# Performance work log

Hardware: AMD Instinct MI355X
Metric: run time of the kernel (lower is better)

## Reference

```python
import jax, jax.numpy as jnp
import numpy as np

D = 1024
H = 16
DK = D // H


def apply_rope(x):
    # x: [B, H, T, dk]; interleaved-pair RoPE as in the torch source
    T, dim = x.shape[-2], x.shape[-1]
    inv_freq = 1.0 / (10000.0 ** (jnp.arange(0, dim, 2, dtype=x.dtype) / dim))  # [dk/2]
    pos = jnp.arange(T, dtype=x.dtype)
    sinusoid = pos[:, None] * inv_freq[None, :]  # [T, dk/2]
    sin, cos = jnp.sin(sinusoid), jnp.cos(sinusoid)
    x1, x2 = x[..., ::2], x[..., 1::2]
    rot = jnp.stack([x1 * cos - x2 * sin, x1 * sin + x2 * cos], axis=-1)
    return rot.reshape(x.shape)


def setup_inputs() -> dict:
    key = jax.random.key(0)
    k1, k2, k3, k4, k5 = jax.random.split(key, 5)
    B, T = 2, 2048
    s = 1.0 / np.sqrt(D)
    return {
        "x": jax.random.normal(k1, (B, T, D), dtype=jnp.float32),
        "W_qkv": jax.random.normal(k2, (D, 3 * D), dtype=jnp.float32) * s,
        "b_qkv": jnp.zeros((3 * D,), dtype=jnp.float32),
        "W_out": jax.random.normal(k3, (D, D), dtype=jnp.float32) * s,
        "b_out": jnp.zeros((D,), dtype=jnp.float32),
    }


def reference(x, W_qkv, b_qkv, W_out, b_out):
    B, T, C = x.shape
    qkv = x @ W_qkv + b_qkv  # [B, T, 3D]
    qkv = qkv.reshape(B, T, 3, H, DK).transpose(2, 0, 3, 1, 4)  # [3, B, H, T, dk]
    q, k, v = qkv[0], qkv[1], qkv[2]
    q, k = apply_rope(q), apply_rope(k)
    scores = jnp.einsum("bhtd,bhsd->bhts", q, k) / jnp.sqrt(jnp.asarray(DK, x.dtype))
    causal = jnp.tril(jnp.ones((T, T), dtype=bool))
    scores = jnp.where(causal, scores, jnp.asarray(-1e9, x.dtype))
    probs = jax.nn.softmax(scores, axis=-1)
    attn = jnp.einsum("bhts,bhsd->bhtd", probs, v)  # [B, H, T, dk]
    out = attn.transpose(0, 2, 1, 3).reshape(B, T, C)  # b h t d -> b t (h d)
    return out @ W_out + b_out
```

## Files before the change

### kernel.cpp

```cpp
#include <hip/hip_runtime.h>
#include <math.h>

#define DMODEL 1024
#define NHEAD  16
#define HDK    64
#define BATCH  2
#define SEQ    2048
#define MROWS  (BATCH*SEQ)
#define NQKV   (3*DMODEL)
#define LOG2_10000 13.287712379549449f
#define INV2PI 0.15915494309189535f
#define SCALE_LOG2E 0.1803368801111137f
#define M_FIX 8.0f

typedef __attribute__((ext_vector_type(8))) short bf16x8;
typedef __attribute__((ext_vector_type(4))) short s16x4;
typedef __attribute__((ext_vector_type(4))) float f32x4;
typedef __attribute__((ext_vector_type(2))) unsigned int u32x2;

__device__ __forceinline__ short f2bf(float f) {
    union { float f; unsigned u; } v; v.f = f;
    unsigned r = v.u + 0x7fffu + ((v.u >> 16) & 1u);
    return (short)(r >> 16);
}

__device__ __forceinline__ float fast_exp2(float x) {
#if __has_builtin(__builtin_amdgcn_exp2f)
    return __builtin_amdgcn_exp2f(x);
#else
    return exp2f(x);
#endif
}

__device__ __forceinline__ void gld_lds16(const short* g, short* l) {
    __builtin_amdgcn_global_load_lds(
        (const __attribute__((address_space(1))) void*)g,
        (__attribute__((address_space(3))) void*)l, 16, 0, 0);
}

__global__ __launch_bounds__(256) void prep_kernel(
    const float* __restrict__ x, const float* __restrict__ wqkv,
    const float* __restrict__ wout,
    short* __restrict__ xb, short* __restrict__ wqkv_t, short* __restrict__ wout_t,
    float2* __restrict__ rope)
{
    __shared__ __align__(16) short tile[32][36];
    const int tid = threadIdx.x;
    if (blockIdx.x < 2048) {
        const int i = (blockIdx.x * 256 + tid) * 8;
        float4 a = *(const float4*)(x + i);
        float4 b = *(const float4*)(x + i + 4);
        bf16x8 o;
        o[0] = f2bf(a.x); o[1] = f2bf(a.y); o[2] = f2bf(a.z); o[3] = f2bf(a.w);
        o[4] = f2bf(b.x); o[5] = f2bf(b.y); o[6] = f2bf(b.z); o[7] = f2bf(b.w);
        *(bf16x8*)(xb + i) = o;
        return;
    }
    if (blockIdx.x >= 2048 + 4096) {
        const int idx = (blockIdx.x - 6144) * 256 + tid;
        const int t = idx >> 5, f = idx & 31;
        const float invf = INV2PI * exp2f(-((float)f / 32.f) * LOG2_10000);
        const float rev = (float)t * invf;
        const float fr = rev - floorf(rev);
        float2 cs;
        cs.x = __builtin_amdgcn_cosf(fr);
        cs.y = __builtin_amdgcn_sinf(fr);
        rope[idx] = cs;
        return;
    }
    const int bx = blockIdx.x - 2048;
    int nx = bx & 127;
    const int ky = bx >> 7;
    const float* in; short* out; int N;
    if (nx < 96) { in = wqkv; out = wqkv_t; N = NQKV; }
    else         { in = wout; out = wout_t; N = DMODEL; nx -= 96; }
    const int n0 = nx * 32, k0 = ky * 32;
    {
        const int kr = tid >> 3, nc4 = tid & 7;
        float4 v = *(const float4*)&in[(size_t)(k0 + kr) * N + n0 + nc4 * 4];
        tile[nc4 * 4 + 0][kr] = f2bf(v.x);
        tile[nc4 * 4 + 1][kr] = f2bf(v.y);
        tile[nc4 * 4 + 2][kr] = f2bf(v.z);
        tile[nc4 * 4 + 3][kr] = f2bf(v.w);
    }
    __syncthreads();
    {
        const int nr = tid >> 3, kc4 = tid & 7;
        *(s16x4*)&out[(size_t)(n0 + nr) * DMODEL + k0 + kc4 * 4] =
            *(const s16x4*)&tile[nr][kc4 * 4];
    }
}

__global__ __launch_bounds__(256) void qkv_gemm_kernel(
    const short* __restrict__ xb, const short* __restrict__ Wt,
    const float* __restrict__ bias, const float2* __restrict__ rope,
    short* __restrict__ qd, short* __restrict__ kd, short* __restrict__ vtb)
{
    __shared__ __align__(16) short As[3][128 * 32];
    __shared__ __align__(16) short Bs[3][128 * 32];
    const int tid = threadIdx.x;
    const int lane = tid & 63, wave = tid >> 6;
    const int wm = wave & 1, wn = wave >> 1;
    const int l15 = lane & 15, quad = lane >> 4;
    const int n0 = blockIdx.x * 128, m0 = blockIdx.y * 128;
    const int srow = lane >> 2, sc = lane & 3;
    const int scp = sc ^ ((srow >> 1) & 3);
    const int rdx = (l15 >> 1) & 3;

    const short* gA1 = xb + (size_t)(m0 + wave * 32 + srow) * DMODEL + scp * 8;
    const short* gA2 = gA1 + (size_t)16 * DMODEL;
    const short* gB1 = Wt + (size_t)(n0 + wave * 32 + srow) * DMODEL + scp * 8;
    const short* gB2 = gB1 + (size_t)16 * DMODEL;
    const int lofsA1 = (wave * 32) * 32;
    const int lofsA2 = (wave * 32 + 16) * 32;

    f32x4 zero = {0.f, 0.f, 0.f, 0.f};
    f32x4 acc[4][4];
    #pragma unroll
    for (int i = 0; i < 4; ++i)
        #pragma unroll
        for (int j = 0; j < 4; ++j) acc[i][j] = zero;

#define QKV_COMPUTE(CUR)                                                          \
    {                                                                             \
        bf16x8 af[4], bfr[4];                                                     \
        _Pragma("unroll")                                                         \
        for (int i = 0; i < 4; ++i)                                               \
            af[i] = *(const bf16x8*)&As[CUR][(wm * 64 + i * 16 + l15) * 32 + (quad ^ rdx) * 8]; \
        _Pragma("unroll")                                                         \
        for (int j = 0; j < 4; ++j)                                               \
            bfr[j] = *(const bf16x8*)&Bs[CUR][(wn * 64 + j * 16 + l15) * 32 + (quad ^ rdx) * 8]; \
        _Pragma("unroll")                                                         \
        for (int i = 0; i < 4; ++i)                                               \
            _Pragma("unroll")                                                     \
            for (int j = 0; j < 4; ++j)                                           \
                acc[i][j] = __builtin_amdgcn_mfma_f32_16x16x32_bf16(af[i], bfr[j], acc[i][j], 0, 0, 0); \
    }

    gld_lds16(gA1, &As[0][lofsA1]);
    gld_lds16(gA2, &As[0][lofsA2]);
    gld_lds16(gB1, &Bs[0][lofsA1]);
    gld_lds16(gB2, &Bs[0][lofsA2]);
    gld_lds16(gA1 + 32, &As[1][lofsA1]);
    gld_lds16(gA2 + 32, &As[1][lofsA2]);
    gld_lds16(gB1 + 32, &Bs[1][lofsA1]);
    gld_lds16(gB2 + 32, &Bs[1][lofsA2]);

    int cur = 0, nx = 2;
    #pragma unroll 3
    for (int k = 0; k < 30; ++k) {
        const int kn = (k + 2) * 32;
        gld_lds16(gA1 + kn, &As[nx][lofsA1]);
        gld_lds16(gA2 + kn, &As[nx][lofsA2]);
        gld_lds16(gB1 + kn, &Bs[nx][lofsA1]);
        gld_lds16(gB2 + kn, &Bs[nx][lofsA2]);
        asm volatile("s_waitcnt vmcnt(8)\n\ts_barrier" ::: "memory");
        QKV_COMPUTE(cur);
        asm volatile("s_barrier" ::: "memory");
        cur = (cur == 2) ? 0 : cur + 1;
        nx  = (nx == 2) ? 0 : nx + 1;
    }
    asm volatile("s_waitcnt vmcnt(4)\n\ts_barrier" ::: "memory");
    QKV_COMPUTE(cur);
    cur = (cur == 2) ? 0 : cur + 1;
    asm volatile("s_waitcnt vmcnt(0)\n\ts_barrier" ::: "memory");
    QKV_COMPUTE(cur);
#undef QKV_COMPUTE

    const int which = n0 >> 10;
    float biasv[4];
    int hh[4], dd[4];
    #pragma unroll
    for (int j = 0; j < 4; ++j) {
        const int n = n0 + wn * 64 + j * 16 + l15;
        biasv[j] = bias[n];
        hh[j] = (n & 1023) >> 6;
        dd[j] = n & 63;
    }
    #pragma unroll
    for (int i = 0; i < 4; ++i) {
        const int mb = m0 + wm * 64 + i * 16 + quad * 4;
        const int b = mb >> 11, tb = mb & (SEQ - 1);
        if (which < 2) {
            #pragma unroll
            for (int j = 0; j < 4; ++j) {
                const int fj = dd[j] >> 1;
                #pragma unroll
                for (int r = 0; r < 4; ++r) {
                    const int t = tb + r;
                    float val = acc[i][j][r] + biasv[j];
                    const float2 cs = rope[t * 32 + fj];
                    const float partner = __shfl_xor(val, 1);
                    val = (lane & 1) ? (partner * cs.y + val * cs.x)
                                     : (val * cs.x - partner * cs.y);
                    short* dst = (which == 0) ? qd : kd;
                    dst[((size_t)(b * NHEAD + hh[j]) * SEQ + t) * HDK + dd[j]] = f2bf(val);
                }
            }
        } else {
            #pragma unroll
            for (int j = 0; j < 4; ++j) {
                s16x4 sv;
                #pragma unroll
                for (int r = 0; r < 4; ++r)
                    sv[r] = f2bf(acc[i][j][r] + biasv[j]);
                *(s16x4*)&vtb[((size_t)(b * NHEAD + hh[j]) * HDK + dd[j]) * SEQ + tb] = sv;
            }
        }
    }
}

__global__ __launch_bounds__(512) void attn_mfma_kernel(
    const short* __restrict__ qd, const short* __restrict__ kd,
    const short* __restrict__ vt, short* __restrict__ od)
{
    __shared__ __align__(16) short Ks[2][2][64 * 32];
    __shared__ __align__(16) short Vs[2][2][64 * 32];
    __shared__ __align__(16) short Ps[8][16 * 64];
    const int tid = threadIdx.x, lane = tid & 63, w = tid >> 6;
    const int l15 = lane & 15, quad = lane >> 4;
    const int par = w >> 2;
    const int ws = w & 3;
    const int id = (int)blockIdx.x;
    const int c = id & 7, g = id >> 3;
    const int qt = 31 - (g >> 2);
    const int jj = g & 3;
    const int hb = c + 8 * jj;
    const int h = hb & 15, b = hb >> 4;
    const size_t base = ((size_t)(b * NHEAD + h)) * SEQ * HDK;
    const int stid = tid & 255;
    const int hi = tid >> 8;
    const int srow = stid >> 2, sc = stid & 3;
    const int lofs = srow * 32 + (sc ^ ((srow >> 1) & 3)) * 8;
    const int rdx = (l15 >> 1) & 3;
    const int pmask = (l15 & 3) << 2;
    f32x4 zero = {0.f, 0.f, 0.f, 0.f};

    const short* kp = kd + base + (size_t)(hi * 64 + srow) * HDK + sc * 8;
    const short* vp = vt + base + (size_t)srow * SEQ + hi * 64 + sc * 8;

    const int q0 = qt * 64;
    const int trow = q0 + ws * 16 + l15;
    bf16x8 qf[2];
    {
        const short* qrow = qd + base + (size_t)trow * HDK;
        qf[0] = *(const bf16x8*)(qrow + quad * 8);
        qf[1] = *(const bf16x8*)(qrow + 32 + quad * 8);
    }
    float l_acc = 0.f;
    f32x4 o[4];
    #pragma unroll
    for (int j = 0; j < 4; ++j) o[j] = zero;

    const int nkt = qt + 1;
    const int npair = (nkt + 1) >> 1;
    short* myPs = &Ps[w][0];

    bf16x8 rk[2], rv[2];
    rk[0] = *(const bf16x8*)kp; rk[1] = *(const bf16x8*)(kp + 32);
    rv[0] = *(const bf16x8*)vp; rv[1] = *(const bf16x8*)(vp + 32);

    for (int p = 0; p < npair; ++p) {
        __syncthreads();
        *(bf16x8*)&Ks[hi][0][lofs] = rk[0];
        *(bf16x8*)&Ks[hi][1][lofs] = rk[1];
        *(bf16x8*)&Vs[hi][0][lofs] = rv[0];
        *(bf16x8*)&Vs[hi][1][lofs] = rv[1];
        __syncthreads();
        if (p + 1 < npair) {
            const int sn = (2 * p + 2) * 64;
            const short* kn = kp + (size_t)sn * HDK;
            const short* vn = vp + sn;
            rk[0] = *(const bf16x8*)kn; rk[1] = *(const bf16x8*)(kn + 32);
            rv[0] = *(const bf16x8*)vn; rv[1] = *(const bf16x8*)(vn + 32);
        }

        const int kt = 2 * p + par;
        if (kt < nkt) {
            f32x4 sacc[4];
            #pragma unroll
            for (int j = 0; j < 4; ++j) {
                const int ro = (j * 16 + l15) * 32 + (quad ^ rdx) * 8;
                bf16x8 kf0 = *(const bf16x8*)&Ks[par][0][ro];
                bf16x8 kf1 = *(const bf16x8*)&Ks[par][1][ro];
                sacc[j] = __builtin_amdgcn_mfma_f32_16x16x32_bf16(kf0, qf[0], zero, 0, 0, 0);
                sacc[j] = __builtin_amdgcn_mfma_f32_16x16x32_bf16(kf1, qf[1], sacc[j], 0, 0, 0);
            }
            if (kt == nkt - 1) {
                const int s0 = kt * 64;
                #pragma unroll
                for (int j = 0; j < 4; ++j) {
                    float pv[4];
                    #pragma unroll
                    for (int r = 0; r < 4; ++r) {
                        const int scol = s0 + j * 16 + quad * 4 + r;
                        const float sv = sacc[j][r] * SCALE_LOG2E - M_FIX;
                        pv[r] = (scol > trow) ? 0.f : fast_exp2(sv);
                        l_acc += pv[r];
                    }
                    unsigned pk0, pk1;
                    asm("v_cvt_pk_bf16_f32 %0, %1, %2" : "=v"(pk0) : "v"(pv[0]), "v"(pv[1]));
                    asm("v_cvt_pk_bf16_f32 %0, %1, %2" : "=v"(pk1) : "v"(pv[2]), "v"(pv[3]));
                    const int cc = (j * 4 + quad) ^ pmask;
                    u32x2 pkv = {pk0, pk1};
                    *(u32x2*)&myPs[l15 * 64 + cc * 4] = pkv;
                }
            } else {
                #pragma unroll
                for (int j = 0; j < 4; ++j) {
                    float pv[4];
                    #pragma unroll
                    for (int r = 0; r < 4; ++r) {
                        pv[r] = fast_exp2(sacc[j][r] * SCALE_LOG2E - M_FIX);
                        l_acc += pv[r];
                    }
                    unsigned pk0, pk1;
                    asm("v_cvt_pk_bf16_f32 %0, %1, %2" : "=v"(pk0) : "v"(pv[0]), "v"(pv[1]));
                    asm("v_cvt_pk_bf16_f32 %0, %1, %2" : "=v"(pk1) : "v"(pv[2]), "v"(pv[3]));
                    const int cc = (j * 4 + quad) ^ pmask;
                    u32x2 pkv = {pk0, pk1};
                    *(u32x2*)&myPs[l15 * 64 + cc * 4] = pkv;
                }
            }
            bf16x8 pf0 = *(const bf16x8*)&myPs[l15 * 64 + ((quad * 2) ^ pmask) * 4];
            bf16x8 pf1 = *(const bf16x8*)&myPs[l15 * 64 + ((8 + quad * 2) ^ pmask) * 4];
            #pragma unroll
            for (int j = 0; j < 4; ++j) {
                const int ro = (j * 16 + l15) * 32 + (quad ^ rdx) * 8;
                bf16x8 vf0 = *(const bf16x8*)&Vs[par][0][ro];
                bf16x8 vf1 = *(const bf16x8*)&Vs[par][1][ro];
                o[j] = __builtin_amdgcn_mfma_f32_16x16x32_bf16(pf0, vf0, o[j], 0, 0, 0);
                o[j] = __builtin_amdgcn_mfma_f32_16x16x32_bf16(pf1, vf1, o[j], 0, 0, 0);
            }
        }
    }

    float sr = l_acc;
    sr += __shfl_xor(sr, 16);
    sr += __shfl_xor(sr, 32);

    __syncthreads();
    float* ob   = (float*)&Ks[0][0][0];
    float* lbuf = (float*)&Vs[0][0][0];
    lbuf[w * 16 + l15] = sr;
    if (par == 1) {
        const int bi = (ws * 64 + lane) * 16;
        #pragma unroll
        for (int j = 0; j < 4; ++j)
            #pragma unroll
            for (int r = 0; r < 4; ++r) ob[bi + j * 4 + r] = o[j][r];
    }
    __syncthreads();
    if (par == 0) {
        const int bi = (ws * 64 + lane) * 16;
        #pragma unroll
        for (int j = 0; j < 4; ++j)
            #pragma unroll
            for (int r = 0; r < 4; ++r) o[j][r] += ob[bi + j * 4 + r];

        #pragma unroll
        for (int r = 0; r < 4; ++r) {
            const int qq = quad * 4 + r;
            const float lt = lbuf[ws * 16 + qq] + lbuf[(ws + 4) * 16 + qq];
            const float inv = 1.f / lt;
            const int t = q0 + ws * 16 + qq;
            #pragma unroll
            for (int j = 0; j < 4; ++j)
                od[((size_t)(b * SEQ + t) * NHEAD + h) * HDK + j * 16 + l15] =
                    f2bf(o[j][r] * inv);
        }
    }
}

__global__ __launch_bounds__(256) void out_gemm_kernel(
    const short* __restrict__ Ab, const short* __restrict__ Wt,
    const float* __restrict__ bias, float* __restrict__ out)
{
    __shared__ __align__(16) short As[2][128 * 32];
    __shared__ __align__(16) short Bs[2][64 * 32];
    const int tid = threadIdx.x;
    const int lane = tid & 63, wave = tid >> 6;
    const int wm = wave & 1, wn = wave >> 1;
    const int l15 = lane & 15, quad = lane >> 4;
    const int n0 = blockIdx.x * 64, m0 = blockIdx.y * 128;
    const int srow = lane >> 2, sc = lane & 3;
    const int scp = sc ^ ((srow >> 1) & 3);
    const int rdx = (l15 >> 1) & 3;

    const short* gA1 = Ab + (size_t)(m0 + wave * 32 + srow) * DMODEL + scp * 8;
    const short* gA2 = gA1 + (size_t)16 * DMODEL;
    const short* gB1 = Wt + (size_t)(n0 + wave * 16 + srow) * DMODEL + scp * 8;
    const int lofsA1 = (wave * 32) * 32;
    const int lofsA2 = (wave * 32 + 16) * 32;
    const int lofsB  = (wave * 16) * 32;

    f32x4 zero = {0.f, 0.f, 0.f, 0.f};
    f32x4 acc[4][2];
    #pragma unroll
    for (int i = 0; i < 4; ++i)
        #pragma unroll
        for (int j = 0; j < 2; ++j) acc[i][j] = zero;

    gld_lds16(gA1, &As[0][lofsA1]);
    gld_lds16(gA2, &As[0][lofsA2]);
    gld_lds16(gB1, &Bs[0][lofsB]);
    __syncthreads();

    for (int k = 0; k < DMODEL / 32; ++k) {
        const int cur = k & 1;
        if (k + 1 < DMODEL / 32) {
            const int kn = (k + 1) * 32;
            gld_lds16(gA1 + kn, &As[cur ^ 1][lofsA1]);
            gld_lds16(gA2 + kn, &As[cur ^ 1][lofsA2]);
            gld_lds16(gB1 + kn, &Bs[cur ^ 1][lofsB]);
        }
        bf16x8 af[4], bfr[2];
        #pragma unroll
        for (int i = 0; i < 4; ++i)
            af[i] = *(const bf16x8*)&As[cur][(wm * 64 + i * 16 + l15) * 32 + (quad ^ rdx) * 8];
        #pragma unroll
        for (int j = 0; j < 2; ++j)
            bfr[j] = *(const bf16x8*)&Bs[cur][(wn * 32 + j * 16 + l15) * 32 + (quad ^ rdx) * 8];
        #pragma unroll
        for (int i = 0; i < 4; ++i)
            #pragma unroll
            for (int j = 0; j < 2; ++j)
                acc[i][j] = __builtin_amdgcn_mfma_f32_16x16x32_bf16(af[i], bfr[j], acc[i][j], 0, 0, 0);
        __syncthreads();
    }

    #pragma unroll
    for (int j = 0; j < 2; ++j) {
        const int n = n0 + wn * 32 + j * 16 + l15;
        const float bv = bias[n];
        #pragma unroll
        for (int i = 0; i < 4; ++i)
            #pragma unroll
            for (int r = 0; r < 4; ++r) {
                const int m = m0 + wm * 64 + i * 16 + quad * 4 + r;
                out[(size_t)m * DMODEL + n] = acc[i][j][r] + bv;
            }
    }
}

extern "C" void kernel_launch(void* const* d_in, const int* in_sizes, int n_in,
                              void* d_out, int out_size, void* d_ws, size_t ws_size,
                              hipStream_t stream) {
    const float* x    = (const float*)d_in[0];
    const float* Wqkv = (const float*)d_in[1];
    const float* bqkv = (const float*)d_in[2];
    const float* Wout = (const float*)d_in[3];
    const float* bout = (const float*)d_in[4];
    float* out = (float*)d_out;

    short* ws = (short*)d_ws;
    short* xb     = ws;
    short* wqkv_t = xb + (size_t)4 * 1024 * 1024;
    short* wout_t = wqkv_t + (size_t)3 * 1024 * 1024;
    short* qd     = wout_t + (size_t)1024 * 1024;
    short* kd     = qd + (size_t)4 * 1024 * 1024;
    short* vtb    = kd + (size_t)4 * 1024 * 1024;
    short* attn   = vtb + (size_t)4 * 1024 * 1024;
    float2* rope  = (float2*)(attn + (size_t)4 * 1024 * 1024);

    prep_kernel<<<2048 + 4096 + 256, 256, 0, stream>>>(
        x, Wqkv, Wout, xb, wqkv_t, wout_t, rope);

    qkv_gemm_kernel<<<dim3(NQKV / 128, MROWS / 128), 256, 0, stream>>>(
        xb, wqkv_t, bqkv, rope, qd, kd, vtb);

    attn_mfma_kernel<<<1024, 512, 0, stream>>>(qd, kd, vtb, attn);

    out_gemm_kernel<<<dim3(DMODEL / 64, MROWS / 128), 256, 0, stream>>>(
        attn, wout_t, bout, out);
}
```

Measured before the change: 185.3 us.

## Widen K tile to 64 with double buffering in QKV and output GEMMs

Result: faster. 181.4 us (-2.1%).

```diff
diff --git a/kernel.cpp b/kernel.cpp
--- a/kernel.cpp
+++ b/kernel.cpp
@@ -96,23 +96,20 @@
     const float* __restrict__ bias, const float2* __restrict__ rope,
     short* __restrict__ qd, short* __restrict__ kd, short* __restrict__ vtb)
 {
-    __shared__ __align__(16) short As[3][128 * 32];
-    __shared__ __align__(16) short Bs[3][128 * 32];
+    __shared__ __align__(16) short As[2][128 * 64];
+    __shared__ __align__(16) short Bs[2][128 * 64];
     const int tid = threadIdx.x;
     const int lane = tid & 63, wave = tid >> 6;
     const int wm = wave & 1, wn = wave >> 1;
     const int l15 = lane & 15, quad = lane >> 4;
     const int n0 = blockIdx.x * 128, m0 = blockIdx.y * 128;
-    const int srow = lane >> 2, sc = lane & 3;
-    const int scp = sc ^ ((srow >> 1) & 3);
-    const int rdx = (l15 >> 1) & 3;
-
-    const short* gA1 = xb + (size_t)(m0 + wave * 32 + srow) * DMODEL + scp * 8;
-    const short* gA2 = gA1 + (size_t)16 * DMODEL;
-    const short* gB1 = Wt + (size_t)(n0 + wave * 32 + srow) * DMODEL + scp * 8;
-    const short* gB2 = gB1 + (size_t)16 * DMODEL;
-    const int lofsA1 = (wave * 32) * 32;
-    const int lofsA2 = (wave * 32 + 16) * 32;
+    const int srow = tid >> 3, sch = tid & 7;
+    const int schg = sch ^ (srow & 7);
+    const int lofs = srow * 64 + sch * 8;
+    const int rsw = l15 & 7;
+
+    const short* gA = xb + (size_t)(m0 + srow) * DMODEL + schg * 8;
+    const short* gB = Wt + (size_t)(n0 + srow) * DMODEL + schg * 8;
 
     f32x4 zero = {0.f, 0.f, 0.f, 0.f};
     f32x4 acc[4][4];
@@ -121,50 +118,52 @@
         #pragma unroll
         for (int j = 0; j < 4; ++j) acc[i][j] = zero;
 
-#define QKV_COMPUTE(CUR)                                                          \
-    {                                                                             \
-        bf16x8 af[4], bfr[4];                                                     \
-        _Pragma("unroll")                                                         \
-        for (int i = 0; i < 4; ++i)                                               \
-            af[i] = *(const bf16x8*)&As[CUR][(wm * 64 + i * 16 + l15) * 32 + (quad ^ rdx) * 8]; \
-        _Pragma("unroll")                                                         \
-        for (int j = 0; j < 4; ++j)                                               \
-            bfr[j] = *(const bf16x8*)&Bs[CUR][(wn * 64 + j * 16 + l15) * 32 + (quad ^ rdx) * 8]; \
-        _Pragma("unroll")                                                         \
-        for (int i = 0; i < 4; ++i)                                               \
-            _Pragma("unroll")                                                     \
-            for (int j = 0; j < 4; ++j)                                           \
-                acc[i][j] = __builtin_amdgcn_mfma_f32_16x16x32_bf16(af[i], bfr[j], acc[i][j], 0, 0, 0); \
-    }
-
-    gld_lds16(gA1, &As[0][lofsA1]);
-    gld_lds16(gA2, &As[0][lofsA2]);
-    gld_lds16(gB1, &Bs[0][lofsA1]);
-    gld_lds16(gB2, &Bs[0][lofsA2]);
-    gld_lds16(gA1 + 32, &As[1][lofsA1]);
-    gld_lds16(gA2 + 32, &As[1][lofsA2]);
-    gld_lds16(gB1 + 32, &Bs[1][lofsA1]);
-    gld_lds16(gB2 + 32, &Bs[1][lofsA2]);
-
-    int cur = 0, nx = 2;
-    #pragma unroll 3
-    for (int k = 0; k < 30; ++k) {
-        const int kn = (k + 2) * 32;
-        gld_lds16(gA1 + kn, &As[nx][lofsA1]);
-        gld_lds16(gA2 + kn, &As[nx][lofsA2]);
-        gld_lds16(gB1 + kn, &Bs[nx][lofsA1]);
-        gld_lds16(gB2 + kn, &Bs[nx][lofsA2]);
-        asm volatile("s_waitcnt vmcnt(8)\n\ts_barrier" ::: "memory");
+#define QKV_STAGE(BUF, KT)                                                     \
+    _Pragma("unroll")                                                          \
+    for (int r_ = 0; r_ < 4; ++r_) {                                           \
+        gld_lds16(gA + (size_t)(KT) * 64 + (size_t)(r_ * 32) * DMODEL,         \
+                  &As[BUF][r_ * 2048 + lofs]);                                 \
+        gld_lds16(gB + (size_t)(KT) * 64 + (size_t)(r_ * 32) * DMODEL,         \
+                  &Bs[BUF][r_ * 2048 + lofs]);                                 \
+    }
+
+#define QKV_COMPUTE(BUF)                                                       \
+    {                                                                          \
+        bf16x8 af[4][2], bfr[4][2];                                            \
+        _Pragma("unroll")                                                      \
+        for (int i = 0; i < 4; ++i) {                                          \
+            const int ra = (wm * 64 + i * 16 + l15) * 64;                      \
+            af[i][0] = *(const bf16x8*)&As[BUF][ra + (quad ^ rsw) * 8];        \
+            af[i][1] = *(const bf16x8*)&As[BUF][ra + ((4 + quad) ^ rsw) * 8];  \
+        }                                                                      \
+        _Pragma("unroll")                                                      \
+        for (int j = 0; j < 4; ++j) {                                          \
+            const int rb = (wn * 64 + j * 16 + l15) * 64;                      \
+            bfr[j][0] = *(const bf16x8*)&Bs[BUF][rb + (quad ^ rsw) * 8];       \
+            bfr[j][1] = *(const bf16x8*)&Bs[BUF][rb + ((4 + quad) ^ rsw) * 8]; \
+        }                                                                      \
+        _Pragma("unroll")                                                      \
+        for (int i = 0; i < 4; ++i)                                            \
+            _Pragma("unroll")                                                  \
+            for (int j = 0; j < 4; ++j) {                                      \
+                acc[i][j] = __builtin_amdgcn_mfma_f32_16x16x32_bf16(           \
+                    af[i][0], bfr[j][0], acc[i][j], 0, 0, 0);                  \
+                acc[i][j] = __builtin_amdgcn_mfma_f32_16x16x32_bf16(           \
+                    af[i][1], bfr[j][1], acc[i][j], 0, 0, 0);                  \
+            }                                                                  \
+    }
+
+    QKV_STAGE(0, 0);
+    asm volatile("s_waitcnt vmcnt(0)\n\ts_barrier" ::: "memory");
+
+    #pragma unroll 2
+    for (int kt = 0; kt < 16; ++kt) {
+        const int cur = kt & 1;
+        if (kt + 1 < 16) QKV_STAGE(cur ^ 1, kt + 1);
         QKV_COMPUTE(cur);
-        asm volatile("s_barrier" ::: "memory");
-        cur = (cur == 2) ? 0 : cur + 1;
-        nx  = (nx == 2) ? 0 : nx + 1;
-    }
-    asm volatile("s_waitcnt vmcnt(4)\n\ts_barrier" ::: "memory");
-    QKV_COMPUTE(cur);
-    cur = (cur == 2) ? 0 : cur + 1;
-    asm volatile("s_waitcnt vmcnt(0)\n\ts_barrier" ::: "memory");
-    QKV_COMPUTE(cur);
+        asm volatile("s_waitcnt vmcnt(0) lgkmcnt(0)\n\ts_barrier" ::: "memory");
+    }
+#undef QKV_STAGE
 #undef QKV_COMPUTE
 
     const int which = n0 >> 10;
@@ -376,23 +375,20 @@
     const short* __restrict__ Ab, const short* __restrict__ Wt,
     const float* __restrict__ bias, float* __restrict__ out)
 {
-    __shared__ __align__(16) short As[2][128 * 32];
-    __shared__ __align__(16) short Bs[2][64 * 32];
+    __shared__ __align__(16) short As[2][128 * 64];
+    __shared__ __align__(16) short Bs[2][64 * 64];
     const int tid = threadIdx.x;
     const int lane = tid & 63, wave = tid >> 6;
     const int wm = wave & 1, wn = wave >> 1;
     const int l15 = lane & 15, quad = lane >> 4;
     const int n0 = blockIdx.x * 64, m0 = blockIdx.y * 128;
-    const int srow = lane >> 2, sc = lane & 3;
-    const int scp = sc ^ ((srow >> 1) & 3);
-    const int rdx = (l15 >> 1) & 3;
-
-    const short* gA1 = Ab + (size_t)(m0 + wave * 32 + srow) * DMODEL + scp * 8;
-    const short* gA2 = gA1 + (size_t)16 * DMODEL;
-    const short* gB1 = Wt + (size_t)(n0 + wave * 16 + srow) * DMODEL + scp * 8;
-    const int lofsA1 = (wave * 32) * 32;
-    const int lofsA2 = (wave * 32 + 16) * 32;
-    const int lofsB  = (wave * 16) * 32;
+    const int srow = tid >> 3, sch = tid & 7;
+    const int schg = sch ^ (srow & 7);
+    const int lofs = srow * 64 + sch * 8;
+    const int rsw = l15 & 7;
+
+    const short* gA = Ab + (size_t)(m0 + srow) * DMODEL + schg * 8;
+    const short* gB = Wt + (size_t)(n0 + srow) * DMODEL + schg * 8;
 
     f32x4 zero = {0.f, 0.f, 0.f, 0.f};
     f32x4 acc[4][2];
@@ -401,33 +397,56 @@
         #pragma unroll
         for (int j = 0; j < 2; ++j) acc[i][j] = zero;
 
-    gld_lds16(gA1, &As[0][lofsA1]);
-    gld_lds16(gA2, &As[0][lofsA2]);
-    gld_lds16(gB1, &Bs[0][lofsB]);
-    __syncthreads();
-
-    for (int k = 0; k < DMODEL / 32; ++k) {
-        const int cur = k & 1;
-        if (k + 1 < DMODEL / 32) {
-            const int kn = (k + 1) * 32;
-            gld_lds16(gA1 + kn, &As[cur ^ 1][lofsA1]);
-            gld_lds16(gA2 + kn, &As[cur ^ 1][lofsA2]);
-            gld_lds16(gB1 + kn, &Bs[cur ^ 1][lofsB]);
-        }
-        bf16x8 af[4], bfr[2];
-        #pragma unroll
-        for (int i = 0; i < 4; ++i)
-            af[i] = *(const bf16x8*)&As[cur][(wm * 64 + i * 16 + l15) * 32 + (quad ^ rdx) * 8];
-        #pragma unroll
-        for (int j = 0; j < 2; ++j)
-            bfr[j] = *(const bf16x8*)&Bs[cur][(wn * 32 + j * 16 + l15) * 32 + (quad ^ rdx) * 8];
-        #pragma unroll
-        for (int i = 0; i < 4; ++i)
-            #pragma unroll
-            for (int j = 0; j < 2; ++j)
-                acc[i][j] = __builtin_amdgcn_mfma_f32_16x16x32_bf16(af[i], bfr[j], acc[i][j], 0, 0, 0);
-        __syncthreads();
-    }
+#define OUT_STAGE(BUF, KT)                                                     \
+    {                                                                          \
+        _Pragma("unroll")                                                      \
+        for (int r_ = 0; r_ < 4; ++r_)                                         \
+            gld_lds16(gA + (size_t)(KT) * 64 + (size_t)(r_ * 32) * DMODEL,     \
+                      &As[BUF][r_ * 2048 + lofs]);                             \
+        _Pragma("unroll")                                                      \
+        for (int r_ = 0; r_ < 2; ++r_)                                         \
+            gld_lds16(gB + (size_t)(KT) * 64 + (size_t)(r_ * 32) * DMODEL,     \
+                      &Bs[BUF][r_ * 2048 + lofs]);                             \
+    }
+
+#define OUT_COMPUTE(BUF)                                                       \
+    {                                                                          \
+        bf16x8 af[4][2], bfr[2][2];                                            \
+        _Pragma("unroll")                                                      \
+        for (int i = 0; i < 4; ++i) {                                          \
+            const int ra = (wm * 64 + i * 16 + l15) * 64;                      \
+            af[i][0] = *(const bf16x8*)&As[BUF][ra + (quad ^ rsw) * 8];        \
+            af[i][1] = *(const bf16x8*)&As[BUF][ra + ((4 + quad) ^ rsw) * 8];  \
+        }                                                                      \
+        _Pragma("unroll")                                                      \
+        for (int j = 0; j < 2; ++j) {                                          \
+            const int rb = (wn * 32 + j * 16 + l15) * 64;                      \
+            bfr[j][0] = *(const bf16x8*)&Bs[BUF][rb + (quad ^ rsw) * 8];       \
+            bfr[j][1] = *(const bf16x8*)&Bs[BUF][rb + ((4 + quad) ^ rsw) * 8]; \
+        }                                                                      \
+        _Pragma("unroll")                                                      \
+        for (int i = 0; i < 4; ++i)                                            \
+            _Pragma("unroll")                                                  \
+            for (int j = 0; j < 2; ++j) {                                      \
+                acc[i][j] = __builtin_amdgcn_mfma_f32_16x16x32_bf16(           \
+                    af[i][0], bfr[j][0], acc[i][j], 0, 0, 0);                  \
+                acc[i][j] = __builtin_amdgcn_mfma_f32_16x16x32_bf16(           \
+                    af[i][1], bfr[j][1], acc[i][j], 0, 0, 0);                  \
+            }                                                                  \
+    }
+
+    OUT_STAGE(0, 0);
+    asm volatile("s_waitcnt vmcnt(0)\n\ts_barrier" ::: "memory");
+
+    #pragma unroll 2
+    for (int kt = 0; kt < 16; ++kt) {
+        const int cur = kt & 1;
+        if (kt + 1 < 16) OUT_STAGE(cur ^ 1, kt + 1);
+        OUT_COMPUTE(cur);
+        asm volatile("s_waitcnt vmcnt(0) lgkmcnt(0)\n\ts_barrier" ::: "memory");
+    }
+#undef OUT_STAGE
+#undef OUT_COMPUTE
 
     #pragma unroll
     for (int j = 0; j < 2; ++j) {
```
